# Kernel optimization log

Hardware: AMD Instinct MI355X
Metric: run time of the kernel (lower is better)

Reference implementation:

```python
import jax, jax.numpy as jnp
import numpy as np

BS, D = 8192, 1024


def setup_inputs() -> dict:
    key = jax.random.key(0)
    k1, k2, k3, k4 = jax.random.split(key, 4)
    return {
        "z": jax.random.normal(k1, (BS, D), dtype=jnp.float32),
        "w": jax.random.normal(k2, (BS, D), dtype=jnp.float32),
        "u": jax.random.normal(k3, (BS, D), dtype=jnp.float32),
        "b": jax.random.normal(k4, (BS,), dtype=jnp.float32),
    }


def reference(z, w, u, b):
    # --- get_batch_corrected_u ---
    wu = jnp.sum(w * u, axis=1)                      # [bs]
    m = -1.0 + jax.nn.softplus(wu)                   # [bs]
    # NOTE: original divides by sqrt of GLOBAL sum over all of w (no axis)
    w_norm = jnp.sqrt(jnp.sum(w ** 2))               # scalar
    u_hat = u + ((m - wu)[:, None] * w) / w_norm     # [bs, d]

    # --- forward transform: diag(tanh(wTz+b)) @ u  ==  tanh(...)[:,None]*u ---
    inner = jnp.sum(w * z, axis=1) + b               # [bs]
    z_new = z + jnp.tanh(inner)[:, None] * u_hat     # [bs, d]

    # --- det_jcb evaluated with UPDATED z (as in the original code) ---
    inner2 = jnp.sum(w * z_new, axis=1) + b          # [bs]
    h_prime = 1.0 - jnp.tanh(inner2) ** 2            # [bs]
    psi_dot_u = h_prime * jnp.sum(u_hat * w, axis=1) # [bs]
    log_det = jnp.log(jnp.abs(1.0 + psi_dot_u))      # [bs]
    return z_new, log_det
```

## Files before the change

kernel.cpp:

```cpp
#include <hip/hip_runtime.h>
#include <math.h>

#define BS   8192
#define D    1024
#define TPB  256
#define NBLK 512
#define RPB  16
#define RPWV 4
#define F4R  4
#define SENT 0xFFFFFFFFu

typedef float floatx4 __attribute__((ext_vector_type(4)));

__global__ __launch_bounds__(TPB, 2) void planar_persistent(
    const float* __restrict__ z, const float* __restrict__ w,
    const float* __restrict__ u, const float* __restrict__ b,
    float* __restrict__ zout, float* __restrict__ ldout,
    unsigned int* __restrict__ partials)
{
    const int t    = threadIdx.x;
    const int wv   = t >> 6;
    const int l    = t & 63;
    const int row0 = blockIdx.x * RPB + wv * RPWV;

    float4 wr[RPWV][F4R];
    float  w2_s[RPWV];
    float  w2acc = 0.f;
#pragma unroll
    for (int r = 0; r < RPWV; ++r) {
        const float4* w4 = (const float4*)w + (size_t)(row0 + r) * (D / 4);
        float w2 = 0.f;
#pragma unroll
        for (int k = 0; k < F4R; ++k) {
            const float4 a = w4[l + (k << 6)];
            wr[r][k] = a;
            w2 += a.x*a.x + a.y*a.y + a.z*a.z + a.w*a.w;
        }
#pragma unroll
        for (int off = 32; off > 0; off >>= 1) w2 += __shfl_xor(w2, off, 64);
        w2_s[r] = w2;
        w2acc  += w2;
    }
    __shared__ float sw[4], sg[4];
    if (l == 0) sw[wv] = w2acc;
    __syncthreads();
    if (t == 0) {
        const float p = sw[0] + sw[1] + sw[2] + sw[3];
        __hip_atomic_store(&partials[blockIdx.x], __float_as_uint(p),
                           __ATOMIC_RELAXED, __HIP_MEMORY_SCOPE_AGENT);
    }

    float4 vr[RPWV][F4R];
    float  wu_s[RPWV], in_s[RPWV], th_s[RPWV];
#pragma unroll
    for (int r = 0; r < RPWV; ++r) {
        const int row = row0 + r;
        const float4* z4 = (const float4*)z + (size_t)row * (D / 4);
        const float4* u4 = (const float4*)u + (size_t)row * (D / 4);
        float4 zv[F4R], uv[F4R];
#pragma unroll
        for (int k = 0; k < F4R; ++k) {
            zv[k] = z4[l + (k << 6)];
            uv[k] = u4[l + (k << 6)];
        }
        float wu = 0.f, wz = 0.f;
#pragma unroll
        for (int k = 0; k < F4R; ++k) {
            const float4 a = wr[r][k];
            wu += a.x*uv[k].x + a.y*uv[k].y + a.z*uv[k].z + a.w*uv[k].w;
            wz += a.x*zv[k].x + a.y*zv[k].y + a.z*zv[k].z + a.w*zv[k].w;
        }
#pragma unroll
        for (int off = 32; off > 0; off >>= 1) {
            wu += __shfl_xor(wu, off, 64);
            wz += __shfl_xor(wz, off, 64);
        }
        const float inner = wz + b[row];
        const float tnh   = tanhf(inner);
#pragma unroll
        for (int k = 0; k < F4R; ++k) {
            vr[r][k].x = fmaf(tnh, uv[k].x, zv[k].x);
            vr[r][k].y = fmaf(tnh, uv[k].y, zv[k].y);
            vr[r][k].z = fmaf(tnh, uv[k].z, zv[k].z);
            vr[r][k].w = fmaf(tnh, uv[k].w, zv[k].w);
        }
        wu_s[r] = wu; in_s[r] = inner; th_s[r] = tnh;
    }

    unsigned int u0, u1;
    for (;;) {
        u0 = __hip_atomic_load(&partials[t], __ATOMIC_RELAXED,
                               __HIP_MEMORY_SCOPE_AGENT);
        u1 = __hip_atomic_load(&partials[t + TPB], __ATOMIC_RELAXED,
                               __HIP_MEMORY_SCOPE_AGENT);
        if (u0 != SENT && u1 != SENT) break;
        __builtin_amdgcn_s_sleep(4);
    }
    float gs = __uint_as_float(u0) + __uint_as_float(u1);
#pragma unroll
    for (int off = 32; off > 0; off >>= 1) gs += __shfl_xor(gs, off, 64);
    if (l == 0) sg[wv] = gs;
    __syncthreads();
    const float wnrm = sqrtf(sg[0] + sg[1] + sg[2] + sg[3]);

#pragma unroll
    for (int r = 0; r < RPWV; ++r) {
        const int   row  = row0 + r;
        const float wu   = wu_s[r];
        const float sp   = (wu > 0.f) ? (wu + log1pf(expf(-wu)))
                                      : log1pf(expf(wu));
        const float coef = (-1.f + sp - wu) / wnrm;
        const float tc   = th_s[r] * coef;
        floatx4* o4 = (floatx4*)zout + (size_t)row * (D / 4);
#pragma unroll
        for (int k = 0; k < F4R; ++k) {
            floatx4 o;
            o.x = fmaf(tc, wr[r][k].x, vr[r][k].x);
            o.y = fmaf(tc, wr[r][k].y, vr[r][k].y);
            o.z = fmaf(tc, wr[r][k].z, vr[r][k].z);
            o.w = fmaf(tc, wr[r][k].w, vr[r][k].w);
            __builtin_nontemporal_store(o, o4 + l + (k << 6));
        }
        if (l == 0) {
            const float s      = fmaf(coef, w2_s[r], wu);
            const float inner2 = fmaf(th_s[r], s, in_s[r]);
            const float th2    = tanhf(inner2);
            const float hp     = 1.f - th2 * th2;
            ldout[row] = logf(fabsf(fmaf(hp, s, 1.f)));
        }
    }
}

extern "C" void kernel_launch(void* const* d_in, const int* in_sizes, int n_in,
                              void* d_out, int out_size, void* d_ws, size_t ws_size,
                              hipStream_t stream) {
    const float* z = (const float*)d_in[0];
    const float* w = (const float*)d_in[1];
    const float* u = (const float*)d_in[2];
    const float* b = (const float*)d_in[3];

    float* out   = (float*)d_out;
    float* zout  = out;
    float* ldout = out + (size_t)BS * D;

    unsigned int* partials = (unsigned int*)d_ws;

    hipMemsetAsync(partials, 0xFF, NBLK * sizeof(unsigned int), stream);
    planar_persistent<<<NBLK, TPB, 0, stream>>>(z, w, u, b, zout, ldout,
                                                partials);
}
```

Measured before the change: 29.79 us.

## Replace memset-sentinel grid barrier with epoch-tagged per-wave slots and hoist loads

```diff
diff --git a/kernel.cpp b/kernel.cpp
--- a/kernel.cpp
+++ b/kernel.cpp
@@ -8,32 +8,58 @@
 #define RPB  16
 #define RPWV 4
 #define F4R  4
-#define SENT 0xFFFFFFFFu
+#define NSLOT (NBLK * 4)
+#define SPT   (NSLOT / TPB)
 
 typedef float floatx4 __attribute__((ext_vector_type(4)));
+typedef unsigned long long u64;
 
 __global__ __launch_bounds__(TPB, 2) void planar_persistent(
     const float* __restrict__ z, const float* __restrict__ w,
     const float* __restrict__ u, const float* __restrict__ b,
     float* __restrict__ zout, float* __restrict__ ldout,
-    unsigned int* __restrict__ partials)
+    u64* __restrict__ slots, unsigned int* __restrict__ epoch)
 {
     const int t    = threadIdx.x;
     const int wv   = t >> 6;
     const int l    = t & 63;
     const int row0 = blockIdx.x * RPB + wv * RPWV;
 
-    float4 wr[RPWV][F4R];
-    float  w2_s[RPWV];
-    float  w2acc = 0.f;
+    const unsigned int e1 =
+        __hip_atomic_load(epoch, __ATOMIC_RELAXED, __HIP_MEMORY_SCOPE_AGENT)
+        + 1u;
+
+    float4 wr[RPWV][F4R], zv[RPWV][F4R], uv[RPWV][F4R];
 #pragma unroll
     for (int r = 0; r < RPWV; ++r) {
         const float4* w4 = (const float4*)w + (size_t)(row0 + r) * (D / 4);
+#pragma unroll
+        for (int k = 0; k < F4R; ++k) wr[r][k] = w4[l + (k << 6)];
+    }
+#pragma unroll
+    for (int r = 0; r < RPWV; ++r) {
+        const float4* z4 = (const float4*)z + (size_t)(row0 + r) * (D / 4);
+#pragma unroll
+        for (int k = 0; k < F4R; ++k) zv[r][k] = z4[l + (k << 6)];
+    }
+#pragma unroll
+    for (int r = 0; r < RPWV; ++r) {
+        const float4* u4 = (const float4*)u + (size_t)(row0 + r) * (D / 4);
+#pragma unroll
+        for (int k = 0; k < F4R; ++k) uv[r][k] = u4[l + (k << 6)];
+    }
+    float brow[RPWV];
+#pragma unroll
+    for (int r = 0; r < RPWV; ++r) brow[r] = b[row0 + r];
+
+    float w2_s[RPWV];
+    float w2acc = 0.f;
+#pragma unroll
+    for (int r = 0; r < RPWV; ++r) {
         float w2 = 0.f;
 #pragma unroll
         for (int k = 0; k < F4R; ++k) {
-            const float4 a = w4[l + (k << 6)];
-            wr[r][k] = a;
+            const float4 a = wr[r][k];
             w2 += a.x*a.x + a.y*a.y + a.z*a.z + a.w*a.w;
         }
 #pragma unroll
@@ -41,67 +67,66 @@
         w2_s[r] = w2;
         w2acc  += w2;
     }
-    __shared__ float sw[4], sg[4];
-    if (l == 0) sw[wv] = w2acc;
-    __syncthreads();
-    if (t == 0) {
-        const float p = sw[0] + sw[1] + sw[2] + sw[3];
-        __hip_atomic_store(&partials[blockIdx.x], __float_as_uint(p),
+    if (l == 0) {
+        const u64 word = ((u64)e1 << 32) | (u64)__float_as_uint(w2acc);
+        __hip_atomic_store(&slots[(blockIdx.x << 2) + wv], word,
                            __ATOMIC_RELAXED, __HIP_MEMORY_SCOPE_AGENT);
     }
 
-    float4 vr[RPWV][F4R];
-    float  wu_s[RPWV], in_s[RPWV], th_s[RPWV];
+    float wu_s[RPWV], in_s[RPWV], th_s[RPWV];
 #pragma unroll
     for (int r = 0; r < RPWV; ++r) {
-        const int row = row0 + r;
-        const float4* z4 = (const float4*)z + (size_t)row * (D / 4);
-        const float4* u4 = (const float4*)u + (size_t)row * (D / 4);
-        float4 zv[F4R], uv[F4R];
-#pragma unroll
-        for (int k = 0; k < F4R; ++k) {
-            zv[k] = z4[l + (k << 6)];
-            uv[k] = u4[l + (k << 6)];
-        }
         float wu = 0.f, wz = 0.f;
 #pragma unroll
         for (int k = 0; k < F4R; ++k) {
             const float4 a = wr[r][k];
-            wu += a.x*uv[k].x + a.y*uv[k].y + a.z*uv[k].z + a.w*uv[k].w;
-            wz += a.x*zv[k].x + a.y*zv[k].y + a.z*zv[k].z + a.w*zv[k].w;
+            wu += a.x*uv[r][k].x + a.y*uv[r][k].y
+                + a.z*uv[r][k].z + a.w*uv[r][k].w;
+            wz += a.x*zv[r][k].x + a.y*zv[r][k].y
+                + a.z*zv[r][k].z + a.w*zv[r][k].w;
         }
 #pragma unroll
         for (int off = 32; off > 0; off >>= 1) {
             wu += __shfl_xor(wu, off, 64);
             wz += __shfl_xor(wz, off, 64);
         }
-        const float inner = wz + b[row];
+        const float inner = wz + brow[r];
         const float tnh   = tanhf(inner);
 #pragma unroll
         for (int k = 0; k < F4R; ++k) {
-            vr[r][k].x = fmaf(tnh, uv[k].x, zv[k].x);
-            vr[r][k].y = fmaf(tnh, uv[k].y, zv[k].y);
-            vr[r][k].z = fmaf(tnh, uv[k].z, zv[k].z);
-            vr[r][k].w = fmaf(tnh, uv[k].w, zv[k].w);
+            zv[r][k].x = fmaf(tnh, uv[r][k].x, zv[r][k].x);
+            zv[r][k].y = fmaf(tnh, uv[r][k].y, zv[r][k].y);
+            zv[r][k].z = fmaf(tnh, uv[r][k].z, zv[r][k].z);
+            zv[r][k].w = fmaf(tnh, uv[r][k].w, zv[r][k].w);
         }
         wu_s[r] = wu; in_s[r] = inner; th_s[r] = tnh;
     }
 
-    unsigned int u0, u1;
+    u64 a[SPT];
     for (;;) {
-        u0 = __hip_atomic_load(&partials[t], __ATOMIC_RELAXED,
-                               __HIP_MEMORY_SCOPE_AGENT);
-        u1 = __hip_atomic_load(&partials[t + TPB], __ATOMIC_RELAXED,
-                               __HIP_MEMORY_SCOPE_AGENT);
-        if (u0 != SENT && u1 != SENT) break;
+        bool ok = true;
+#pragma unroll
+        for (int i = 0; i < SPT; ++i) {
+            a[i] = __hip_atomic_load(&slots[t + i * TPB], __ATOMIC_RELAXED,
+                                     __HIP_MEMORY_SCOPE_AGENT);
+            ok = ok && ((unsigned int)(a[i] >> 32) == e1);
+        }
+        if (ok) break;
         __builtin_amdgcn_s_sleep(4);
     }
-    float gs = __uint_as_float(u0) + __uint_as_float(u1);
+    float gs = 0.f;
+#pragma unroll
+    for (int i = 0; i < SPT; ++i) gs += __uint_as_float((unsigned int)a[i]);
 #pragma unroll
     for (int off = 32; off > 0; off >>= 1) gs += __shfl_xor(gs, off, 64);
+    __shared__ float sg[4];
     if (l == 0) sg[wv] = gs;
     __syncthreads();
     const float wnrm = sqrtf(sg[0] + sg[1] + sg[2] + sg[3]);
+
+    if (blockIdx.x == 0 && t == 0)
+        __hip_atomic_store(epoch, e1, __ATOMIC_RELEASE,
+                           __HIP_MEMORY_SCOPE_AGENT);
 
 #pragma unroll
     for (int r = 0; r < RPWV; ++r) {
@@ -115,10 +140,10 @@
 #pragma unroll
         for (int k = 0; k < F4R; ++k) {
             floatx4 o;
-            o.x = fmaf(tc, wr[r][k].x, vr[r][k].x);
-            o.y = fmaf(tc, wr[r][k].y, vr[r][k].y);
-            o.z = fmaf(tc, wr[r][k].z, vr[r][k].z);
-            o.w = fmaf(tc, wr[r][k].w, vr[r][k].w);
+            o.x = fmaf(tc, wr[r][k].x, zv[r][k].x);
+            o.y = fmaf(tc, wr[r][k].y, zv[r][k].y);
+            o.z = fmaf(tc, wr[r][k].z, zv[r][k].z);
+            o.w = fmaf(tc, wr[r][k].w, zv[r][k].w);
             __builtin_nontemporal_store(o, o4 + l + (k << 6));
         }
         if (l == 0) {
@@ -143,9 +168,9 @@
     float* zout  = out;
     float* ldout = out + (size_t)BS * D;
 
-    unsigned int* partials = (unsigned int*)d_ws;
+    u64*          slots = (u64*)d_ws;
+    unsigned int* epoch = (unsigned int*)(slots + NSLOT);
 
-    hipMemsetAsync(partials, 0xFF, NBLK * sizeof(unsigned int), stream);
     planar_persistent<<<NBLK, TPB, 0, stream>>>(z, w, u, b, zout, ldout,
-                                                partials);
+                                                slots, epoch);
 }
```

After: 32.49 us. 1.09x slower.
